# Kernel optimization log

Measured on AMD Instinct MI355X. Metric: run time of the kernel, lower is better.

The kernel has to match this reference:

```python
import jax, jax.numpy as jnp
import numpy as np

STRIDE = 1
PADDING = 1

def setup_inputs() -> dict:
    key = jax.random.key(0)
    k1, k2 = jax.random.split(key)
    x = jax.random.normal(k1, (32, 128, 56, 56), dtype=jnp.float32)
    weight = jax.random.normal(k2, (256, 128, 3, 3), dtype=jnp.float32) * 0.01
    bias = jnp.zeros((256,), dtype=jnp.float32)
    return {"x": x, "weight": weight, "bias": bias}

def reference(x, weight, bias):
    # Same math as unfold (im2col) + matmul conv: a standard 2D cross-correlation.
    # Expressed as lax.conv_general_dilated, the efficient implicit-GEMM form.
    out = jax.lax.conv_general_dilated(
        x, weight,
        window_strides=(STRIDE, STRIDE),
        padding=[(PADDING, PADDING), (PADDING, PADDING)],
        dimension_numbers=("NCHW", "OIHW", "NCHW"),
    )
    out = out + bias[None, :, None, None]
    return out
```

## Files before the change

kernel.cpp:

```cpp
#include <hip/hip_runtime.h>

typedef int   v4i __attribute__((ext_vector_type(4)));
typedef float v4f __attribute__((ext_vector_type(4)));
typedef unsigned short ushort_t;

#define NB 32
#define CI 128
#define HW 56
#define KOC 256
#define HP 58
#define MTOT (NB*HW*HW)
#define XP_ELEMS ((size_t)NB*HP*HP*CI)
#define XP_OFF_BYTES ((size_t)1<<20)

__device__ __forceinline__ unsigned short f2bf(float f) {
    unsigned int u = __builtin_bit_cast(unsigned int, f);
    u += 0x7fffu + ((u >> 16) & 1u);
    return (unsigned short)(u >> 16);
}

__device__ __forceinline__ void gload16(const void* g, void* l) {
    __builtin_amdgcn_global_load_lds(
        (const __attribute__((address_space(1))) void*)g,
        (__attribute__((address_space(3))) void*)l, 16, 0, 0);
}

__global__ void wt_bf16(const float* __restrict__ w, ushort_t* __restrict__ wb) {
    int t = blockIdx.x * 256 + threadIdx.x;
    if (t >= KOC * CI) return;
    const float* src = w + (size_t)t * 9;
    int ko = t >> 7, c = t & 127;
    #pragma unroll
    for (int rs = 0; rs < 9; ++rs)
        wb[(size_t)(rs * KOC + ko) * CI + c] = f2bf(src[rs]);
}

__global__ void pad_nhwc_bf16(const float* __restrict__ x, ushort_t* __restrict__ xp) {
    __shared__ ushort_t tile[HW][136];
    int b = blockIdx.x;
    int n = b / HW, h = b % HW;
    int tid = threadIdx.x;
    const float* xr = x + (size_t)n * CI * HW * HW + (size_t)h * HW;
    for (int idx = tid; idx < CI * HW; idx += 256) {
        int c = idx / HW, w = idx % HW;
        tile[w][c] = f2bf(xr[(size_t)c * (HW * HW) + w]);
    }
    __syncthreads();
    ushort_t* xpr = xp + ((size_t)(n * HP + (h + 1)) * HP + 1) * CI;
    for (int idx = tid; idx < (HW * CI) / 8; idx += 256) {
        int w = idx >> 4, c8 = (idx & 15) * 8;
        *reinterpret_cast<uint4*>(xpr + (size_t)w * CI + c8) =
            *reinterpret_cast<const uint4*>(&tile[w][c8]);
    }
}

__global__ void border_zero(ushort_t* __restrict__ xp) {
    int t = blockIdx.x * 256 + threadIdx.x;
    if (t >= NB * 228 * 16) return;
    int c16 = t & 15;
    int p = (t >> 4) % 228;
    int n = t / (228 * 16);
    int h, wc;
    if (p < 58)       { h = 0;               wc = p; }
    else if (p < 116) { h = 57;              wc = p - 58; }
    else { int q = p - 116; h = 1 + (q >> 1); wc = (q & 1) * 57; }
    size_t off = ((size_t)(n * HP + h) * HP + wc) * CI + (size_t)c16 * 8;
    uint4 z; z.x = z.y = z.z = z.w = 0u;
    *reinterpret_cast<uint4*>(xp + off) = z;
}


__global__ __launch_bounds__(256, 4) void conv_mfma(
    const ushort_t* __restrict__ xp,
    const ushort_t* __restrict__ wb,
    const float* __restrict__ bias,
    float* __restrict__ out)
{
    __shared__ alignas(16) ushort_t sA[128 * 32];
    __shared__ alignas(16) ushort_t sB[128 * 32];

    const int tid  = threadIdx.x;
    const int lane = tid & 63;
    const int wv   = tid >> 6;
    const int wko  = wv >> 1, wm = wv & 1;
    const int bid   = blockIdx.x;
    const int chunk = (bid & 7) * 196 + (bid >> 3);
    const int mt = chunk >> 1, kt = chunk & 1;
    const int m0 = mt * 128, ko0 = kt * 128;
    const int lm = lane & 15, lk = lane >> 4;

    const int sc   = (lane & 3) ^ ((lane >> 3) & 3);
    const int row0 = wv * 16 + (lane >> 2);
    const size_t wS0 = (size_t)(ko0 + row0) * CI + sc * 8;
    const size_t wS1 = (size_t)(ko0 + 64 + row0) * CI + sc * 8;
    size_t xS0, xS1;
    {
        int mm = m0 + row0;
        int n = mm / 3136, tt = mm % 3136, oh = tt / 56, ow = tt % 56;
        xS0 = ((size_t)(n * HP + oh) * HP + ow) * CI + sc * 8;
        mm = m0 + 64 + row0;
        n = mm / 3136; tt = mm % 3136; oh = tt / 56; ow = tt % 56;
        xS1 = ((size_t)(n * HP + oh) * HP + ow) * CI + sc * 8;
    }

    int aoffE[4], boffE[4];
    #pragma unroll
    for (int a = 0; a < 4; ++a) {
        int row = wko * 64 + a * 16 + lm;
        aoffE[a] = row * 32 + (lk ^ ((row >> 1) & 3)) * 8;
    }
    #pragma unroll
    for (int b = 0; b < 4; ++b) {
        int row = wm * 64 + b * 16 + lm;
        boffE[b] = row * 32 + (lk ^ ((row >> 1) & 3)) * 8;
    }

    v4f acc[4][4];
    const v4f vzero = {0.f, 0.f, 0.f, 0.f};
    #pragma unroll
    for (int a = 0; a < 4; ++a)
        #pragma unroll
        for (int b = 0; b < 4; ++b) acc[a][b] = vzero;

    char* dA = (char*)sA + wv * 1024;
    char* dB = (char*)sB + wv * 1024;

    for (int it = 0; it < 36; ++it) {
        int rs = it >> 2, coff = (it & 3) * 32;
        int r  = (rs * 11) >> 5, s = rs - r * 3;
        size_t woff = (size_t)rs * (KOC * CI) + coff;
        size_t xoff = (size_t)(r * HP + s) * CI + coff;

        gload16(wb + wS0 + woff, dA);
        gload16(wb + wS1 + woff, dA + 4096);
        gload16(xp + xS0 + xoff, dB);
        gload16(xp + xS1 + xoff, dB + 4096);
        __syncthreads();

        v4i af[4], bf[4];
        #pragma unroll
        for (int a = 0; a < 4; ++a)
            af[a] = *reinterpret_cast<const v4i*>(&sA[aoffE[a]]);
        #pragma unroll
        for (int b = 0; b < 4; ++b)
            bf[b] = *reinterpret_cast<const v4i*>(&sB[boffE[b]]);

        __builtin_amdgcn_s_setprio(1);
        #pragma unroll
        for (int a = 0; a < 4; ++a)
            #pragma unroll
            for (int b = 0; b < 4; ++b)
                asm volatile("v_mfma_f32_16x16x32_bf16 %0, %1, %2, %0"
                             : "+v"(acc[a][b]) : "v"(af[a]), "v"(bf[b]));
        __builtin_amdgcn_s_setprio(0);
        __syncthreads();
    }

    asm volatile("s_nop 7\n\ts_nop 7\n\ts_nop 7"
        : "+v"(acc[0][0]), "+v"(acc[0][1]), "+v"(acc[0][2]), "+v"(acc[0][3]),
          "+v"(acc[1][0]), "+v"(acc[1][1]), "+v"(acc[1][2]), "+v"(acc[1][3]),
          "+v"(acc[2][0]), "+v"(acc[2][1]), "+v"(acc[2][2]), "+v"(acc[2][3]),
          "+v"(acc[3][0]), "+v"(acc[3][1]), "+v"(acc[3][2]), "+v"(acc[3][3]));

    const int koB = ko0 + wko * 64 + lk * 4;
    v4f bv[4];
    #pragma unroll
    for (int a = 0; a < 4; ++a)
        bv[a] = *reinterpret_cast<const v4f*>(bias + koB + a * 16);

    #pragma unroll
    for (int bb = 0; bb < 4; ++bb) {
        int mcol = m0 + wm * 64 + bb * 16 + lm;
        int n = mcol / 3136, t4 = mcol % 3136, oh = t4 / 56, ow = t4 % 56;
        size_t obase = (size_t)n * (KOC * 3136) + (size_t)oh * 56 + ow;
        #pragma unroll
        for (int a = 0; a < 4; ++a) {
            int kk = koB + a * 16;
            #pragma unroll
            for (int r = 0; r < 4; ++r)
                out[obase + (size_t)(kk + r) * 3136] = acc[a][bb][r] + bv[a][r];
        }
    }
}

__global__ void conv_naive(const float* __restrict__ x, const float* __restrict__ w,
                           const float* __restrict__ bias, float* __restrict__ out) {
    int idx = blockIdx.x * 256 + threadIdx.x;
    if (idx >= NB * KOC * HW * HW) return;
    int ow = idx % 56, t = idx / 56, oh = t % 56, t2 = t / 56, ko = t2 % 256, n = t2 / 256;
    float accv = bias[ko];
    for (int c = 0; c < CI; ++c)
        for (int r = 0; r < 3; ++r) {
            int ih = oh - 1 + r;
            if (ih < 0 || ih >= HW) continue;
            for (int s = 0; s < 3; ++s) {
                int iw = ow - 1 + s;
                if (iw < 0 || iw >= HW) continue;
                accv += x[((size_t)(n * CI + c) * HW + ih) * HW + iw] *
                        w[((size_t)(ko * CI + c) * 3 + r) * 3 + s];
            }
        }
    out[idx] = accv;
}

extern "C" void kernel_launch(void* const* d_in, const int* in_sizes, int n_in,
                              void* d_out, int out_size, void* d_ws, size_t ws_size,
                              hipStream_t stream) {
    const float* x    = (const float*)d_in[0];
    const float* w    = (const float*)d_in[1];
    const float* bias = (const float*)d_in[2];
    float* out = (float*)d_out;

    size_t need = XP_OFF_BYTES + XP_ELEMS * 2;
    if (ws_size < need) {
        int tot = NB * KOC * HW * HW;
        conv_naive<<<dim3((tot + 255) / 256), dim3(256), 0, stream>>>(x, w, bias, out);
        return;
    }

    ushort_t* wbp = (ushort_t*)d_ws;
    ushort_t* xpd = (ushort_t*)((char*)d_ws + XP_OFF_BYTES);

    border_zero<<<dim3((NB * 228 * 16 + 255) / 256), dim3(256), 0, stream>>>(xpd);
    wt_bf16<<<dim3((KOC * CI + 255) / 256), dim3(256), 0, stream>>>(w, wbp);
    pad_nhwc_bf16<<<dim3(NB * HW), dim3(256), 0, stream>>>(x, xpd);

    conv_mfma<<<dim3((MTOT / 128) * 2), dim3(256), 0, stream>>>(xpd, wbp, bias, out);
}
```

Before: 105.2 us.

## Double-buffer weight tiles in LDS and load activations directly into registers

The main loop now double-buffers only the weight (A) tile in LDS, prefetching the next iteration's weights while the current MFMAs run. Activation (B) fragments are loaded straight from global memory into registers with inline-asm global_load_dwordx4, which removes the activation LDS staging and one barrier per iteration. The loop is unrolled in pairs with manual vmcnt/lgkmcnt waits. The risks are more VGPR pressure and uncoalesced per-lane activation reads that no longer go through shared memory. Correctness also depends on the hand-placed waitcnt ordering.

```diff
diff --git a/kernel.cpp b/kernel.cpp
--- a/kernel.cpp
+++ b/kernel.cpp
@@ -70,14 +70,49 @@
 }
 
 
+#define BODY(POFF, VM, DO_STAGE, IT) do {                                         \
+    const int it_ = (IT);                                                         \
+    const int rs_ = it_ >> 2;                                                     \
+    const int r_ = (rs_ * 11) >> 5, s_ = rs_ - r_ * 3;                            \
+    const unsigned xstep = (unsigned)(((r_ * HP + s_) * CI + (it_ & 3) * 32) * 2);\
+    _Pragma("unroll")                                                             \
+    for (int b = 0; b < 4; ++b)                                                   \
+        asm volatile("global_load_dwordx4 %0, %1, %2"                             \
+                     : "=v"(bf[b]) : "v"(xoff[b] + xstep), "s"(xp));              \
+    if (DO_STAGE) {                                                               \
+        const int itn = it_ + 1;                                                  \
+        const int rsn = itn >> 2;                                                 \
+        const size_t woffn = (size_t)rsn * (KOC * CI) + (itn & 3) * 32;           \
+        char* dst = (char*)&sA[0][0] + ((POFF) ^ 8192) + wv * 1024;               \
+        gload16(wb + wS0 + woffn, dst);                                           \
+        gload16(wb + wS1 + woffn, dst + 4096);                                    \
+    }                                                                             \
+    _Pragma("unroll")                                                             \
+    for (int a = 0; a < 4; ++a)                                                   \
+        asm volatile("ds_read_b128 %0, %1 offset:" #POFF                          \
+                     : "=v"(af[a]) : "v"(aAddr[a]));                              \
+    asm volatile("s_waitcnt vmcnt(" #VM ")");                                     \
+    asm volatile("s_waitcnt lgkmcnt(0)");                                         \
+    __builtin_amdgcn_sched_barrier(0);                                            \
+    __builtin_amdgcn_s_setprio(1);                                                \
+    _Pragma("unroll")                                                             \
+    for (int a = 0; a < 4; ++a)                                                   \
+        _Pragma("unroll")                                                         \
+        for (int b = 0; b < 4; ++b)                                               \
+            asm volatile("v_mfma_f32_16x16x32_bf16 %0, %1, %2, %0"                \
+                         : "+v"(acc[a][b]) : "v"(af[a]), "v"(bf[b]));             \
+    __builtin_amdgcn_s_setprio(0);                                                \
+    asm volatile("s_waitcnt vmcnt(0)");                                           \
+    __builtin_amdgcn_s_barrier();                                                 \
+} while (0)
+
 __global__ __launch_bounds__(256, 4) void conv_mfma(
     const ushort_t* __restrict__ xp,
     const ushort_t* __restrict__ wb,
     const float* __restrict__ bias,
     float* __restrict__ out)
 {
-    __shared__ alignas(16) ushort_t sA[128 * 32];
-    __shared__ alignas(16) ushort_t sB[128 * 32];
+    __shared__ alignas(16) ushort_t sA[2][4096];
 
     const int tid  = threadIdx.x;
     const int lane = tid & 63;
@@ -93,26 +128,21 @@
     const int row0 = wv * 16 + (lane >> 2);
     const size_t wS0 = (size_t)(ko0 + row0) * CI + sc * 8;
     const size_t wS1 = (size_t)(ko0 + 64 + row0) * CI + sc * 8;
-    size_t xS0, xS1;
-    {
-        int mm = m0 + row0;
-        int n = mm / 3136, tt = mm % 3136, oh = tt / 56, ow = tt % 56;
-        xS0 = ((size_t)(n * HP + oh) * HP + ow) * CI + sc * 8;
-        mm = m0 + 64 + row0;
-        n = mm / 3136; tt = mm % 3136; oh = tt / 56; ow = tt % 56;
-        xS1 = ((size_t)(n * HP + oh) * HP + ow) * CI + sc * 8;
-    }
-
-    int aoffE[4], boffE[4];
+
+    unsigned aAddr[4];
     #pragma unroll
     for (int a = 0; a < 4; ++a) {
         int row = wko * 64 + a * 16 + lm;
-        aoffE[a] = row * 32 + (lk ^ ((row >> 1) & 3)) * 8;
-    }
+        aAddr[a] = (unsigned)(size_t)&sA[0][0]
+                 + (unsigned)(row * 64 + (lk ^ ((row >> 1) & 3)) * 16);
+    }
+
+    unsigned xoff[4];
     #pragma unroll
     for (int b = 0; b < 4; ++b) {
-        int row = wm * 64 + b * 16 + lm;
-        boffE[b] = row * 32 + (lk ^ ((row >> 1) & 3)) * 8;
+        int mm = m0 + wm * 64 + b * 16 + lm;
+        int n = mm / 3136, tt = mm % 3136, oh = tt / 56, ow = tt % 56;
+        xoff[b] = (unsigned)((((size_t)(n * HP + oh) * HP + ow) * CI + lk * 8) * 2);
     }
 
     v4f acc[4][4];
@@ -122,39 +152,22 @@
         #pragma unroll
         for (int b = 0; b < 4; ++b) acc[a][b] = vzero;
 
-    char* dA = (char*)sA + wv * 1024;
-    char* dB = (char*)sB + wv * 1024;
-
-    for (int it = 0; it < 36; ++it) {
-        int rs = it >> 2, coff = (it & 3) * 32;
-        int r  = (rs * 11) >> 5, s = rs - r * 3;
-        size_t woff = (size_t)rs * (KOC * CI) + coff;
-        size_t xoff = (size_t)(r * HP + s) * CI + coff;
-
-        gload16(wb + wS0 + woff, dA);
-        gload16(wb + wS1 + woff, dA + 4096);
-        gload16(xp + xS0 + xoff, dB);
-        gload16(xp + xS1 + xoff, dB + 4096);
-        __syncthreads();
-
-        v4i af[4], bf[4];
-        #pragma unroll
-        for (int a = 0; a < 4; ++a)
-            af[a] = *reinterpret_cast<const v4i*>(&sA[aoffE[a]]);
-        #pragma unroll
-        for (int b = 0; b < 4; ++b)
-            bf[b] = *reinterpret_cast<const v4i*>(&sB[boffE[b]]);
-
-        __builtin_amdgcn_s_setprio(1);
-        #pragma unroll
-        for (int a = 0; a < 4; ++a)
-            #pragma unroll
-            for (int b = 0; b < 4; ++b)
-                asm volatile("v_mfma_f32_16x16x32_bf16 %0, %1, %2, %0"
-                             : "+v"(acc[a][b]) : "v"(af[a]), "v"(bf[b]));
-        __builtin_amdgcn_s_setprio(0);
-        __syncthreads();
-    }
+    v4i af[4], bf[4];
+
+    {
+        char* dst = (char*)&sA[0][0] + wv * 1024;
+        gload16(wb + wS0, dst);
+        gload16(wb + wS1, dst + 4096);
+    }
+    asm volatile("s_waitcnt vmcnt(0)");
+    __builtin_amdgcn_s_barrier();
+
+    for (int t = 0; t < 17; ++t) {
+        BODY(0,    2, true, 2 * t);
+        BODY(8192, 2, true, 2 * t + 1);
+    }
+    BODY(0,    2, true,  34);
+    BODY(8192, 0, false, 35);
 
     asm volatile("s_nop 7\n\ts_nop 7\n\ts_nop 7"
         : "+v"(acc[0][0]), "+v"(acc[0][1]), "+v"(acc[0][2]), "+v"(acc[0][3]),
```

Measured after the change: 163.9 us. 55.8% more time.
